# Kernel optimization log

Hardware: AMD Instinct MI355X
Metric: run time of the kernel (lower is better)

The kernel has to match this reference:

```python
import jax, jax.numpy as jnp
import numpy as np

DIM = 2048
INTER = 1408          # moe_inter_dim per routed expert
N_EXPERTS = 32
TOPK = 6
N_GROUPS = 8
TOPK_GROUPS = 4
ROUTE_SCALE = 2.5
SHARED_INTER = 2816   # n_shared_experts(2) * moe_inter_dim
T = 8192              # tokens (batch*seq flattened)
INIT = 0.02


def setup_inputs() -> dict:
    key = jax.random.key(0)
    k = jax.random.split(key, 8)
    x = jax.random.normal(k[0], (T, DIM), jnp.float32)
    gate_w = jax.random.normal(k[1], (N_EXPERTS, DIM), jnp.float32) * INIT
    # stacked routed-expert weights (torch Linear convention: [out, in])
    w1 = jax.random.normal(k[2], (N_EXPERTS, INTER, DIM), jnp.float32) * INIT
    w2 = jax.random.normal(k[3], (N_EXPERTS, DIM, INTER), jnp.float32) * INIT
    w3 = jax.random.normal(k[4], (N_EXPERTS, INTER, DIM), jnp.float32) * INIT
    # shared experts (single fused MLP, inter = n_shared * moe_inter_dim)
    sw1 = jax.random.normal(k[5], (SHARED_INTER, DIM), jnp.float32) * INIT
    sw2 = jax.random.normal(k[6], (DIM, SHARED_INTER), jnp.float32) * INIT
    sw3 = jax.random.normal(k[7], (SHARED_INTER, DIM), jnp.float32) * INIT
    return {"x": x, "gate_w": gate_w, "w1": w1, "w2": w2, "w3": w3,
            "sw1": sw1, "sw2": sw2, "sw3": sw3}


def _gate(x, gate_w):
    # sigmoid scores, no bias (dim != 7168), group-limited top-k routing
    scores = jax.nn.sigmoid(x @ gate_w.T)                  # (T, E)
    original = scores
    sg = scores.reshape(x.shape[0], N_GROUPS, -1)          # (T, G, E/G)
    group_scores = sg.max(axis=-1)                         # (T, G)  (amax branch)
    _, gidx = jax.lax.top_k(group_scores, TOPK_GROUPS)     # (T, Gk)
    gmask = jnp.zeros((x.shape[0], N_GROUPS), bool).at[
        jnp.arange(x.shape[0])[:, None], gidx].set(True)
    masked = jnp.where(gmask[:, :, None], sg, 0.0).reshape(x.shape[0], -1)
    _, idx = jax.lax.top_k(masked, TOPK)                   # (T, K)
    w = jnp.take_along_axis(original, idx, axis=1)         # gather pre-mask scores
    w = w / w.sum(axis=-1, keepdims=True)                  # sigmoid normalization
    w = w * ROUTE_SCALE
    return w.astype(x.dtype), idx


def reference(x, gate_w, w1, w2, w3, sw1, sw2, sw3):
    weights, idx = _gate(x, gate_w)                        # (T,K), (T,K) int
    # per-token combine weight for each expert: cw[t,e] = sum_k w[t,k]*[idx==e]
    onehot = jax.nn.one_hot(idx, N_EXPERTS, dtype=weights.dtype)  # (T,K,E)
    cw = jnp.einsum('tk,tke->et', weights, onehot)         # (E, T)

    def expert_step(acc, ew):
        W1, W2, W3, cwe = ew                               # cwe: (T,)
        h = jax.nn.silu(x @ W1.T) * (x @ W3.T)             # (T, INTER)
        return acc + cwe[:, None] * (h @ W2.T), None

    y, _ = jax.lax.scan(expert_step, jnp.zeros_like(x), (w1, w2, w3, cw))
    # shared experts MLP (SwiGLU)
    z = (jax.nn.silu(x @ sw1.T) * (x @ sw3.T)) @ sw2.T
    return y + z
```

## Files before the change

### kernel.cpp

```cpp
#include <hip/hip_runtime.h>
#include <hip/hip_bf16.h>
#include <stdint.h>

typedef unsigned short u16;

#define T_TOK 8192
#define DIM 2048
#define INTER 1408
#define NEXP 32
#define TOPK 6
#define SHINTER 2816
#define SLOTS (T_TOK * TOPK)

typedef __attribute__((ext_vector_type(8))) short bf16x8;
typedef __attribute__((ext_vector_type(4))) float f32x4;

__device__ inline u16 f2bf(float f) {
  union { float f; unsigned u; } c; c.f = f;
  unsigned r = (c.u + 0x7FFFu + ((c.u >> 16) & 1u)) >> 16;
  return (u16)r;
}
__device__ inline float bf2f(u16 h) {
  union { unsigned u; float f; } c; c.u = ((unsigned)h) << 16;
  return c.f;
}

__device__ __forceinline__ void gl16(const void* g, void* l) {
  __builtin_amdgcn_global_load_lds(
      (const __attribute__((address_space(1))) void*)g,
      (__attribute__((address_space(3))) void*)l, 16, 0, 0);
}

__global__ __launch_bounds__(256)
void gate_route_k(const float* __restrict__ x, const float* __restrict__ gw,
                  int* __restrict__ tidx, float* __restrict__ tw, int* __restrict__ counts)
{
  int lane = threadIdx.x & 63, w = threadIdx.x >> 6;
  int t = blockIdx.x * 4 + w;
  __shared__ float sc[4][32];
  __shared__ float gm[4][8];
  const float* xr = x + (size_t)t * DIM + lane * 4;
  float4 xv[8];
#pragma unroll
  for (int i = 0; i < 8; i++) xv[i] = *(const float4*)(xr + i * 256);
  for (int e = 0; e < NEXP; e++) {
    const float* g = gw + (size_t)e * DIM + lane * 4;
    float acc = 0.f;
#pragma unroll
    for (int i = 0; i < 8; i++) {
      float4 gv = *(const float4*)(g + i * 256);
      acc += xv[i].x * gv.x + xv[i].y * gv.y + xv[i].z * gv.z + xv[i].w * gv.w;
    }
#pragma unroll
    for (int off = 32; off > 0; off >>= 1) acc += __shfl_down(acc, off);
    if (lane == 0) sc[w][e] = 1.f / (1.f + __expf(-acc));
  }
  if (lane == 0) {
#pragma unroll
    for (int g = 0; g < 8; g++)
      gm[w][g] = fmaxf(fmaxf(sc[w][g*4+0], sc[w][g*4+1]), fmaxf(sc[w][g*4+2], sc[w][g*4+3]));
    unsigned gsel = 0u;
    for (int it = 0; it < 4; it++) {
      float best = -1.f; int bi = 0;
      for (int g = 0; g < 8; g++)
        if (!((gsel >> g) & 1u) && gm[w][g] > best) { best = gm[w][g]; bi = g; }
      gsel |= 1u << bi;
    }
    unsigned chosen = 0u; float wsum = 0.f;
    int ids[TOPK]; float wv[TOPK];
#pragma unroll
    for (int it = 0; it < TOPK; it++) {
      float best = -1.f; int bi = 0;
      for (int e = 0; e < NEXP; e++)
        if (((gsel >> (e >> 2)) & 1u) && !((chosen >> e) & 1u) && sc[w][e] > best) { best = sc[w][e]; bi = e; }
      chosen |= 1u << bi; ids[it] = bi; wv[it] = best; wsum += best;
    }
    float s = 2.5f / wsum;
#pragma unroll
    for (int k = 0; k < TOPK; k++) {
      tidx[t * TOPK + k] = ids[k];
      tw[t * TOPK + k] = wv[k] * s;
      atomicAdd(&counts[ids[k]], 1);
    }
  }
}

__global__ void zero32(int* p) { if (threadIdx.x < NEXP) p[threadIdx.x] = 0; }

__global__ void scan_desc_k(const int* __restrict__ counts, int* __restrict__ offs,
                            int4* __restrict__ desc, int* __restrict__ ntiles)
{
  if (threadIdx.x != 0 || blockIdx.x != 0) return;
  int off = 0, n = 0;
  for (int e = 0; e < NEXP; e++) {
    offs[e] = off;
    int c = counts[e];
    int nt = (c + 127) >> 7;
    for (int i = 0; i < nt; i++) {
      int rem = c - i * 128;
      desc[n] = make_int4(e, off + i * 128, rem < 128 ? rem : 128, 0);
      n++;
    }
    off += c;
  }
  offs[NEXP] = off;
  ntiles[0] = n;
}

__global__ __launch_bounds__(256)
void perm_build_k(const int* __restrict__ tidx, const float* __restrict__ tw,
                  const int* __restrict__ offs, int* __restrict__ ptok,
                  float* __restrict__ pw, int* __restrict__ slotof)
{
  int e = blockIdx.x;
  int tid = threadIdx.x, lane = tid & 63, w = tid >> 6;
  __shared__ int wsum[4];
  __shared__ int cursor;
  if (tid == 0) cursor = offs[e];
  __syncthreads();
  for (int start = 0; start < SLOTS; start += 256) {
    int i = start + tid;
    int match = (tidx[i] == e) ? 1 : 0;
    unsigned long long b = __ballot(match);
    if (lane == 0) wsum[w] = __popcll(b);
    __syncthreads();
    int base = cursor;
    int waveoff = 0;
    for (int ww = 0; ww < w; ww++) waveoff += wsum[ww];
    int total = wsum[0] + wsum[1] + wsum[2] + wsum[3];
    if (match) {
      int before = __popcll(b & ((1ull << lane) - 1ull));
      int slot = base + waveoff + before;
      ptok[slot] = i / TOPK;
      pw[slot] = tw[i];
      slotof[i] = slot;
    }
    __syncthreads();
    if (tid == 0) cursor = base + total;
  }
}

__global__ __launch_bounds__(256)
void cvt_w_k(const float* __restrict__ src, u16* __restrict__ dst, int n8)
{
  int stride = gridDim.x * 256;
  for (size_t i = (size_t)blockIdx.x * 256 + threadIdx.x; i < (size_t)n8; i += stride) {
    size_t j = i * 8;
    float4 a = *(const float4*)(src + j);
    float4 b = *(const float4*)(src + j + 4);
    union { u16 h[8]; uint4 u; } p;
    p.h[0] = f2bf(a.x); p.h[1] = f2bf(a.y); p.h[2] = f2bf(a.z); p.h[3] = f2bf(a.w);
    p.h[4] = f2bf(b.x); p.h[5] = f2bf(b.y); p.h[6] = f2bf(b.z); p.h[7] = f2bf(b.w);
    *(uint4*)(dst + j) = p.u;
  }
}


template<bool SHARED>
__global__ __launch_bounds__(256, 2)
void up2_k(const u16* __restrict__ xb,
           const u16* __restrict__ B1g, const u16* __restrict__ B3g,
           const int* __restrict__ ptok,
           const int4* __restrict__ desc, const int* __restrict__ ntiles,
           u16* __restrict__ Hout)
{
  constexpr int HLD = SHARED ? SHINTER : INTER;
  int row_tile = blockIdx.x, col_tile = blockIdx.y;
  int slot_base, rows;
  const u16 *B1, *B3;
  if constexpr (SHARED) { slot_base = row_tile * 128; rows = 128; B1 = B1g; B3 = B3g; }
  else {
    if (row_tile >= ntiles[0]) return;
    int4 d = desc[row_tile];
    slot_base = d.y; rows = d.z;
    size_t off = (size_t)d.x * (size_t)INTER * DIM;
    B1 = B1g + off; B3 = B3g + off;
  }
  int n0 = col_tile * 128;
  int tid = threadIdx.x, lane = tid & 63;
  int w = tid >> 6, wr = w >> 1, wc = w & 1;

  __shared__ u16 As[128][64];
  __shared__ u16 Bs1[128][64];
  __shared__ u16 Bs3[128][64];

  int selem = (((lane & 7) ^ (lane >> 3)) * 8);
  const u16 *a_src[4], *b1_src[4], *b3_src[4];
#pragma unroll
  for (int s = 0; s < 4; s++) {
    int r = w * 32 + s * 8 + (lane >> 3);
    int tok;
    if constexpr (SHARED) tok = slot_base + r;
    else { int rr = r < rows ? r : rows - 1; tok = ptok[slot_base + rr]; }
    a_src[s]  = xb + (size_t)tok * DIM + selem;
    b1_src[s] = B1 + (size_t)(n0 + r) * DIM + selem;
    b3_src[s] = B3 + (size_t)(n0 + r) * DIM + selem;
  }

  f32x4 acc1[4][4], acc3[4][4];
#pragma unroll
  for (int m = 0; m < 4; m++)
#pragma unroll
    for (int n = 0; n < 4; n++) { acc1[m][n] = {0.f,0.f,0.f,0.f}; acc3[m][n] = {0.f,0.f,0.f,0.f}; }

  for (int kk = 0; kk < DIM / 64; kk++) {
    __syncthreads();
#pragma unroll
    for (int s = 0; s < 4; s++) {
      gl16(a_src[s]  + kk * 64, &As [w * 32 + s * 8][0]);
      gl16(b1_src[s] + kk * 64, &Bs1[w * 32 + s * 8][0]);
      gl16(b3_src[s] + kk * 64, &Bs3[w * 32 + s * 8][0]);
    }
    __syncthreads();
#pragma unroll
    for (int h = 0; h < 2; h++) {
      bf16x8 af[4], b1f[4], b3f[4];
      int chk = (h * 4 + (lane >> 4)) ^ (lane & 7);
#pragma unroll
      for (int m = 0; m < 4; m++)
        af[m] = *(const bf16x8*)&As[wr * 64 + m * 16 + (lane & 15)][chk * 8];
#pragma unroll
      for (int n = 0; n < 4; n++) {
        b1f[n] = *(const bf16x8*)&Bs1[wc * 64 + n * 16 + (lane & 15)][chk * 8];
        b3f[n] = *(const bf16x8*)&Bs3[wc * 64 + n * 16 + (lane & 15)][chk * 8];
      }
#pragma unroll
      for (int m = 0; m < 4; m++)
#pragma unroll
        for (int n = 0; n < 4; n++) {
          acc1[m][n] = __builtin_amdgcn_mfma_f32_16x16x32_bf16(af[m], b1f[n], acc1[m][n], 0, 0, 0);
          acc3[m][n] = __builtin_amdgcn_mfma_f32_16x16x32_bf16(af[m], b3f[n], acc3[m][n], 0, 0, 0);
        }
    }
  }
#pragma unroll
  for (int m = 0; m < 4; m++) {
#pragma unroll
    for (int r = 0; r < 4; r++) {
      int row_local = wr * 64 + m * 16 + (lane >> 4) * 4 + r;
      if (row_local < rows) {
        size_t rowp = (size_t)(slot_base + row_local) * HLD + n0 + wc * 64 + (lane & 15);
#pragma unroll
        for (int n = 0; n < 4; n++) {
          float c1 = acc1[m][n][r], c3 = acc3[m][n][r];
          float hval = (c1 / (1.f + __expf(-c1))) * c3;
          Hout[rowp + n * 16] = f2bf(hval);
        }
      }
    }
  }
}

template<bool SHARED>
__global__ __launch_bounds__(256, 2)
void down2_k(const u16* __restrict__ Hin, const u16* __restrict__ Bg,
             const int4* __restrict__ desc, const int* __restrict__ ntiles,
             const float* __restrict__ pw,
             u16* __restrict__ slotout, float* __restrict__ yout)
{
  constexpr int KD = SHARED ? SHINTER : INTER;
  constexpr int KSTEPS = KD / 64;
  int row_tile = blockIdx.x, col_tile = blockIdx.y;
  int slot_base, rows; const u16* B;
  if constexpr (SHARED) { slot_base = row_tile * 128; rows = 128; B = Bg; }
  else {
    if (row_tile >= ntiles[0]) return;
    int4 d = desc[row_tile]; slot_base = d.y; rows = d.z;
    B = Bg + (size_t)d.x * DIM * INTER;
  }
  int n0 = col_tile * 128;
  int tid = threadIdx.x, lane = tid & 63;
  int w = tid >> 6, wr = w >> 1, wc = w & 1;
  __shared__ u16 As[128][64];
  __shared__ u16 Bs[128][64];

  int selem = (((lane & 7) ^ (lane >> 3)) * 8);
  const u16 *a_src[4], *b_src[4];
#pragma unroll
  for (int s = 0; s < 4; s++) {
    int r = w * 32 + s * 8 + (lane >> 3);
    a_src[s] = Hin + (size_t)(slot_base + r) * KD + selem;
    b_src[s] = B + (size_t)(n0 + r) * KD + selem;
  }

  f32x4 acc[4][4];
#pragma unroll
  for (int m = 0; m < 4; m++)
#pragma unroll
    for (int n = 0; n < 4; n++) acc[m][n] = {0.f,0.f,0.f,0.f};

  for (int kk = 0; kk < KSTEPS; kk++) {
    __syncthreads();
#pragma unroll
    for (int s = 0; s < 4; s++) {
      gl16(a_src[s] + kk * 64, &As[w * 32 + s * 8][0]);
      gl16(b_src[s] + kk * 64, &Bs[w * 32 + s * 8][0]);
    }
    __syncthreads();
#pragma unroll
    for (int h = 0; h < 2; h++) {
      bf16x8 af[4], bfv[4];
      int chk = (h * 4 + (lane >> 4)) ^ (lane & 7);
#pragma unroll
      for (int m = 0; m < 4; m++)
        af[m] = *(const bf16x8*)&As[wr * 64 + m * 16 + (lane & 15)][chk * 8];
#pragma unroll
      for (int n = 0; n < 4; n++)
        bfv[n] = *(const bf16x8*)&Bs[wc * 64 + n * 16 + (lane & 15)][chk * 8];
#pragma unroll
      for (int m = 0; m < 4; m++)
#pragma unroll
        for (int n = 0; n < 4; n++)
          acc[m][n] = __builtin_amdgcn_mfma_f32_16x16x32_bf16(af[m], bfv[n], acc[m][n], 0, 0, 0);
    }
  }
#pragma unroll
  for (int m = 0; m < 4; m++) {
#pragma unroll
    for (int r = 0; r < 4; r++) {
      int row_local = wr * 64 + m * 16 + (lane >> 4) * 4 + r;
      if (row_local < rows) {
        int slot = slot_base + row_local;
        size_t rp = (size_t)slot * DIM + n0 + wc * 64 + (lane & 15);
        if constexpr (SHARED) {
#pragma unroll
          for (int n = 0; n < 4; n++) yout[rp + n * 16] = acc[m][n][r];
        } else {
          float sw = pw[slot];
#pragma unroll
          for (int n = 0; n < 4; n++) slotout[rp + n * 16] = f2bf(acc[m][n][r] * sw);
        }
      }
    }
  }
}

template<bool SHARED>
__global__ __launch_bounds__(256, 2)
void up_gemm_k(const u16* __restrict__ xb,
               const float* __restrict__ W1g, const float* __restrict__ W3g,
               const int* __restrict__ ptok,
               const int4* __restrict__ desc, const int* __restrict__ ntiles,
               u16* __restrict__ Hout)
{
  constexpr int HLD = SHARED ? SHINTER : INTER;
  int row_tile = blockIdx.x, col_tile = blockIdx.y;
  int slot_base, rows;
  const float *B1, *B3;
  if constexpr (SHARED) {
    slot_base = row_tile * 128; rows = 128; B1 = W1g; B3 = W3g;
  } else {
    if (row_tile >= ntiles[0]) return;
    int4 d = desc[row_tile];
    slot_base = d.y; rows = d.z;
    size_t off = (size_t)d.x * (size_t)INTER * DIM;
    B1 = W1g + off; B3 = W3g + off;
  }
  int n0 = col_tile * 128;
  int tid = threadIdx.x, lane = tid & 63;
  int wv = tid >> 6, wr = wv >> 1, wc = wv & 1;

  __shared__ u16 As[128][72];
  __shared__ u16 Bs1[128][72];
  __shared__ u16 Bs3[128][72];

  int ar = tid >> 3, ac = (tid & 7) * 8;
  const u16* asrc[4];
#pragma unroll
  for (int s = 0; s < 4; s++) {
    int r = s * 32 + ar;
    int tok;
    if constexpr (SHARED) tok = slot_base + r;
    else { int rr = r < rows ? r : rows - 1; tok = ptok[slot_base + rr]; }
    asrc[s] = xb + (size_t)tok * DIM + ac;
  }
  int br = tid >> 4, bc = (tid & 15) * 4;
  const float* b1p = B1 + (size_t)(n0 + br) * DIM + bc;
  const float* b3p = B3 + (size_t)(n0 + br) * DIM + bc;

  f32x4 acc1[4][4], acc3[4][4];
#pragma unroll
  for (int m = 0; m < 4; m++)
#pragma unroll
    for (int n = 0; n < 4; n++) { acc1[m][n] = {0.f,0.f,0.f,0.f}; acc3[m][n] = {0.f,0.f,0.f,0.f}; }

  for (int kk = 0; kk < DIM / 64; kk++) {
    __syncthreads();
#pragma unroll
    for (int s = 0; s < 4; s++) {
      uint4 v = *(const uint4*)(asrc[s] + kk * 64);
      *(uint4*)&As[s * 32 + ar][ac] = v;
    }
#pragma unroll
    for (int s = 0; s < 8; s++) {
      float4 v = *(const float4*)(b1p + (size_t)(s * 16) * DIM + kk * 64);
      union { u16 h[4]; uint2 q; } o;
      o.h[0] = f2bf(v.x); o.h[1] = f2bf(v.y); o.h[2] = f2bf(v.z); o.h[3] = f2bf(v.w);
      *(uint2*)&Bs1[s * 16 + br][bc] = o.q;
    }
#pragma unroll
    for (int s = 0; s < 8; s++) {
      float4 v = *(const float4*)(b3p + (size_t)(s * 16) * DIM + kk * 64);
      union { u16 h[4]; uint2 q; } o;
      o.h[0] = f2bf(v.x); o.h[1] = f2bf(v.y); o.h[2] = f2bf(v.z); o.h[3] = f2bf(v.w);
      *(uint2*)&Bs3[s * 16 + br][bc] = o.q;
    }
    __syncthreads();
#pragma unroll
    for (int h = 0; h < 2; h++) {
      bf16x8 af[4], b1f[4], b3f[4];
#pragma unroll
      for (int m = 0; m < 4; m++)
        af[m] = *(const bf16x8*)&As[wr * 64 + m * 16 + (lane & 15)][h * 32 + (lane >> 4) * 8];
#pragma unroll
      for (int n = 0; n < 4; n++) {
        b1f[n] = *(const bf16x8*)&Bs1[wc * 64 + n * 16 + (lane & 15)][h * 32 + (lane >> 4) * 8];
        b3f[n] = *(const bf16x8*)&Bs3[wc * 64 + n * 16 + (lane & 15)][h * 32 + (lane >> 4) * 8];
      }
#pragma unroll
      for (int m = 0; m < 4; m++)
#pragma unroll
        for (int n = 0; n < 4; n++) {
          acc1[m][n] = __builtin_amdgcn_mfma_f32_16x16x32_bf16(af[m], b1f[n], acc1[m][n], 0, 0, 0);
          acc3[m][n] = __builtin_amdgcn_mfma_f32_16x16x32_bf16(af[m], b3f[n], acc3[m][n], 0, 0, 0);
        }
    }
  }
#pragma unroll
  for (int m = 0; m < 4; m++) {
#pragma unroll
    for (int r = 0; r < 4; r++) {
      int row_local = wr * 64 + m * 16 + (lane >> 4) * 4 + r;
      if (row_local < rows) {
        size_t rowp = (size_t)(slot_base + row_local) * HLD + n0 + wc * 64 + (lane & 15);
#pragma unroll
        for (int n = 0; n < 4; n++) {
          float c1 = acc1[m][n][r], c3 = acc3[m][n][r];
          float hval = (c1 / (1.f + __expf(-c1))) * c3;
          Hout[rowp + n * 16] = f2bf(hval);
        }
      }
    }
  }
}

template<bool SHARED>
__global__ __launch_bounds__(256, 2)
void down_gemm_k(const u16* __restrict__ Hin, const float* __restrict__ Bg,
                 const int4* __restrict__ desc, const int* __restrict__ ntiles,
                 const float* __restrict__ pw,
                 u16* __restrict__ slotout, float* __restrict__ yout)
{
  constexpr int KD = SHARED ? SHINTER : INTER;
  constexpr int KSTEPS = KD / 64;
  int row_tile = blockIdx.x, col_tile = blockIdx.y;
  int slot_base, rows; const float* B;
  if constexpr (SHARED) { slot_base = row_tile * 128; rows = 128; B = Bg; }
  else {
    if (row_tile >= ntiles[0]) return;
    int4 d = desc[row_tile]; slot_base = d.y; rows = d.z;
    B = Bg + (size_t)d.x * DIM * INTER;
  }
  int n0 = col_tile * 128;
  int tid = threadIdx.x, lane = tid & 63;
  int wv = tid >> 6, wr = wv >> 1, wc = wv & 1;
  __shared__ u16 As[128][72];
  __shared__ u16 Bs[128][72];
  int ar = tid >> 3, ac = (tid & 7) * 8;
  const u16* asrc[4];
#pragma unroll
  for (int s = 0; s < 4; s++)
    asrc[s] = Hin + (size_t)(slot_base + s * 32 + ar) * KD + ac;
  int br = tid >> 4, bc = (tid & 15) * 4;
  const float* bp = B + (size_t)(n0 + br) * KD + bc;

  f32x4 acc[4][4];
#pragma unroll
  for (int m = 0; m < 4; m++)
#pragma unroll
    for (int n = 0; n < 4; n++) acc[m][n] = {0.f,0.f,0.f,0.f};

  for (int kk = 0; kk < KSTEPS; kk++) {
    __syncthreads();
#pragma unroll
    for (int s = 0; s < 4; s++) {
      uint4 v = *(const uint4*)(asrc[s] + kk * 64);
      *(uint4*)&As[s * 32 + ar][ac] = v;
    }
#pragma unroll
    for (int s = 0; s < 8; s++) {
      float4 v = *(const float4*)(bp + (size_t)(s * 16) * KD + kk * 64);
      union { u16 h[4]; uint2 q; } o;
      o.h[0] = f2bf(v.x); o.h[1] = f2bf(v.y); o.h[2] = f2bf(v.z); o.h[3] = f2bf(v.w);
      *(uint2*)&Bs[s * 16 + br][bc] = o.q;
    }
    __syncthreads();
#pragma unroll
    for (int h = 0; h < 2; h++) {
      bf16x8 af[4], bfv[4];
#pragma unroll
      for (int m = 0; m < 4; m++)
        af[m] = *(const bf16x8*)&As[wr * 64 + m * 16 + (lane & 15)][h * 32 + (lane >> 4) * 8];
#pragma unroll
      for (int n = 0; n < 4; n++)
        bfv[n] = *(const bf16x8*)&Bs[wc * 64 + n * 16 + (lane & 15)][h * 32 + (lane >> 4) * 8];
#pragma unroll
      for (int m = 0; m < 4; m++)
#pragma unroll
        for (int n = 0; n < 4; n++)
          acc[m][n] = __builtin_amdgcn_mfma_f32_16x16x32_bf16(af[m], bfv[n], acc[m][n], 0, 0, 0);
    }
  }
#pragma unroll
  for (int m = 0; m < 4; m++) {
#pragma unroll
    for (int r = 0; r < 4; r++) {
      int row_local = wr * 64 + m * 16 + (lane >> 4) * 4 + r;
      if (row_local < rows) {
        int slot = slot_base + row_local;
        size_t rp = (size_t)slot * DIM + n0 + wc * 64 + (lane & 15);
        if constexpr (SHARED) {
#pragma unroll
          for (int n = 0; n < 4; n++) yout[rp + n * 16] = acc[m][n][r];
        } else {
          float sw = pw[slot];
#pragma unroll
          for (int n = 0; n < 4; n++) slotout[rp + n * 16] = f2bf(acc[m][n][r] * sw);
        }
      }
    }
  }
}

__global__ __launch_bounds__(256)
void combine_k(float* __restrict__ y, const u16* __restrict__ slotout, const int* __restrict__ slotof)
{
  int t = blockIdx.x;
  int c = threadIdx.x * 8;
  size_t rp = (size_t)t * DIM + c;
  float4 a = *(const float4*)(y + rp);
  float4 b = *(const float4*)(y + rp + 4);
  float o[8] = {a.x, a.y, a.z, a.w, b.x, b.y, b.z, b.w};
#pragma unroll
  for (int k = 0; k < TOPK; k++) {
    int s = slotof[t * TOPK + k];
    uint4 v = *(const uint4*)(slotout + (size_t)s * DIM + c);
    o[0] += bf2f((u16)(v.x & 0xFFFFu)); o[1] += bf2f((u16)(v.x >> 16));
    o[2] += bf2f((u16)(v.y & 0xFFFFu)); o[3] += bf2f((u16)(v.y >> 16));
    o[4] += bf2f((u16)(v.z & 0xFFFFu)); o[5] += bf2f((u16)(v.z >> 16));
    o[6] += bf2f((u16)(v.w & 0xFFFFu)); o[7] += bf2f((u16)(v.w >> 16));
  }
  *(float4*)(y + rp)     = make_float4(o[0], o[1], o[2], o[3]);
  *(float4*)(y + rp + 4) = make_float4(o[4], o[5], o[6], o[7]);
}

extern "C" void kernel_launch(void* const* d_in, const int* in_sizes, int n_in,
                              void* d_out, int out_size, void* d_ws, size_t ws_size,
                              hipStream_t stream)
{
  const float* x   = (const float*)d_in[0];
  const float* gw  = (const float*)d_in[1];
  const float* w1  = (const float*)d_in[2];
  const float* w2  = (const float*)d_in[3];
  const float* w3  = (const float*)d_in[4];
  const float* sw1 = (const float*)d_in[5];
  const float* sw2 = (const float*)d_in[6];
  const float* sw3 = (const float*)d_in[7];
  float* y = (float*)d_out;
  char* ws = (char*)d_ws;

  int*   counts = (int*)(ws + 0);
  int*   ntiles = (int*)(ws + 256);
  int*   offs   = (int*)(ws + 512);
  int4*  desc   = (int4*)(ws + 768);
  int*   tidx   = (int*)(ws + 8192);
  float* tw     = (float*)(ws + 204800);
  int*   ptok   = (int*)(ws + 401408);
  float* pw     = (float*)(ws + 598016);
  int*   slotof = (int*)(ws + 794624);
  u16*   xb     = (u16*)(ws + 991232);
  u16*   H      = (u16*)(ws + 34545664ull);
  u16*   Hs     = (u16*)(ws + 173318144ull);
  u16*   sout   = (u16*)(ws + 219455488ull);
  u16*   w1b    = (u16*)(ws + 420782080ull);
  u16*   w3b    = (u16*)(ws + 605331456ull);
  u16*   w2b    = (u16*)(ws + 789880832ull);
  u16*   sw1b   = (u16*)(ws + 974430208ull);
  u16*   sw3b   = (u16*)(ws + 985964544ull);
  u16*   sw2b   = (u16*)(ws + 997498880ull);
  const unsigned long long NEED_FULL = 1009033216ull;

  zero32<<<1, 64, 0, stream>>>(counts);
  gate_route_k<<<2048, 256, 0, stream>>>(x, gw, tidx, tw, counts);
  cvt_w_k<<<2048, 256, 0, stream>>>(x, xb, T_TOK * DIM / 8);
  scan_desc_k<<<1, 64, 0, stream>>>(counts, offs, desc, ntiles);
  perm_build_k<<<32, 256, 0, stream>>>(tidx, tw, offs, ptok, pw, slotof);

  if (ws_size >= NEED_FULL) {
    const int NW = NEXP * INTER * DIM / 8;
    const int NS = SHINTER * DIM / 8;
    cvt_w_k<<<4096, 256, 0, stream>>>(w1,  w1b,  NW);
    cvt_w_k<<<4096, 256, 0, stream>>>(w3,  w3b,  NW);
    cvt_w_k<<<4096, 256, 0, stream>>>(w2,  w2b,  NW);
    cvt_w_k<<<1024, 256, 0, stream>>>(sw1, sw1b, NS);
    cvt_w_k<<<1024, 256, 0, stream>>>(sw3, sw3b, NS);
    cvt_w_k<<<1024, 256, 0, stream>>>(sw2, sw2b, NS);

    up2_k<false><<<dim3(416, 11), 256, 0, stream>>>(xb, w1b, w3b, ptok, desc, ntiles, H);
    up2_k<true ><<<dim3(64, 22), 256, 0, stream>>>(xb, sw1b, sw3b, ptok, desc, ntiles, Hs);
    down2_k<true ><<<dim3(64, 16), 256, 0, stream>>>(Hs, sw2b, desc, ntiles, pw, sout, y);
    down2_k<false><<<dim3(416, 16), 256, 0, stream>>>(H, w2b, desc, ntiles, pw, sout, y);
  } else {
    up_gemm_k<false><<<dim3(416, 11), 256, 0, stream>>>(xb, w1, w3, ptok, desc, ntiles, H);
    up_gemm_k<true ><<<dim3(64, 22), 256, 0, stream>>>(xb, sw1, sw3, ptok, desc, ntiles, Hs);
    down_gemm_k<true ><<<dim3(64, 16), 256, 0, stream>>>(Hs, sw2, desc, ntiles, pw, sout, y);
    down_gemm_k<false><<<dim3(416, 16), 256, 0, stream>>>(H, w2, desc, ntiles, pw, sout, y);
  }

  combine_k<<<8192, 256, 0, stream>>>(y, sout, slotof);
}
```

Measured before the change: 2.487 ms.

## Parallelize scan, widen perm build, raise GEMM occupancy, remap row tiles across XCDs

The expert-offset scan moves from one serial thread to wave-wide shuffle prefix sums, and the permutation builder uses 1024-thread blocks. The grouped GEMM kernels raise the launch-bounds occupancy hint from 2 to 3 blocks per CU. They also permute blockIdx.x so that consecutive row tiles land on the same XCD, with the aim of improving L2 reuse of expert weights. The higher occupancy hint may force register spills, and the tile remap relies on gridDim.x being divisible by 8.

```diff
diff --git a/kernel.cpp b/kernel.cpp
--- a/kernel.cpp
+++ b/kernel.cpp
@@ -88,37 +88,50 @@
 __global__ void zero32(int* p) { if (threadIdx.x < NEXP) p[threadIdx.x] = 0; }
 
 __global__ void scan_desc_k(const int* __restrict__ counts, int* __restrict__ offs,
-                            int4* __restrict__ desc, int* __restrict__ ntiles)
-{
-  if (threadIdx.x != 0 || blockIdx.x != 0) return;
-  int off = 0, n = 0;
-  for (int e = 0; e < NEXP; e++) {
-    offs[e] = off;
-    int c = counts[e];
-    int nt = (c + 127) >> 7;
+                            int4* __restrict__ desc128, int* __restrict__ ntiles)
+{
+  int lane = threadIdx.x;
+  int c = (lane < NEXP) ? counts[lane] : 0;
+  int inc = c;
+#pragma unroll
+  for (int d = 1; d < 64; d <<= 1) {
+    int v = __shfl_up(inc, d);
+    if (lane >= d) inc += v;
+  }
+  int off_e = inc - c;
+  int nt = (c + 127) >> 7;
+  int tinc = nt;
+#pragma unroll
+  for (int d = 1; d < 64; d <<= 1) {
+    int v = __shfl_up(tinc, d);
+    if (lane >= d) tinc += v;
+  }
+  int tex = tinc - nt;
+  if (lane < NEXP) {
+    offs[lane] = off_e;
     for (int i = 0; i < nt; i++) {
       int rem = c - i * 128;
-      desc[n] = make_int4(e, off + i * 128, rem < 128 ? rem : 128, 0);
-      n++;
-    }
-    off += c;
-  }
-  offs[NEXP] = off;
-  ntiles[0] = n;
-}
-
-__global__ __launch_bounds__(256)
+      desc128[tex + i] = make_int4(lane, off_e + i * 128, rem < 128 ? rem : 128, 0);
+    }
+  }
+  if (lane == NEXP - 1) {
+    offs[NEXP] = inc;
+    ntiles[0] = tinc;
+  }
+}
+
+__global__ __launch_bounds__(1024)
 void perm_build_k(const int* __restrict__ tidx, const float* __restrict__ tw,
                   const int* __restrict__ offs, int* __restrict__ ptok,
                   float* __restrict__ pw, int* __restrict__ slotof)
 {
   int e = blockIdx.x;
   int tid = threadIdx.x, lane = tid & 63, w = tid >> 6;
-  __shared__ int wsum[4];
+  __shared__ int wsum[16];
   __shared__ int cursor;
   if (tid == 0) cursor = offs[e];
   __syncthreads();
-  for (int start = 0; start < SLOTS; start += 256) {
+  for (int start = 0; start < SLOTS; start += 1024) {
     int i = start + tid;
     int match = (tidx[i] == e) ? 1 : 0;
     unsigned long long b = __ballot(match);
@@ -127,7 +140,9 @@
     int base = cursor;
     int waveoff = 0;
     for (int ww = 0; ww < w; ww++) waveoff += wsum[ww];
-    int total = wsum[0] + wsum[1] + wsum[2] + wsum[3];
+    int total = 0;
+#pragma unroll
+    for (int ww = 0; ww < 16; ww++) total += wsum[ww];
     if (match) {
       int before = __popcll(b & ((1ull << lane) - 1ull));
       int slot = base + waveoff + before;
@@ -157,7 +172,7 @@
 
 
 template<bool SHARED>
-__global__ __launch_bounds__(256, 2)
+__global__ __launch_bounds__(256, 3)
 void up2_k(const u16* __restrict__ xb,
            const u16* __restrict__ B1g, const u16* __restrict__ B3g,
            const int* __restrict__ ptok,
@@ -165,7 +180,9 @@
            u16* __restrict__ Hout)
 {
   constexpr int HLD = SHARED ? SHINTER : INTER;
-  int row_tile = blockIdx.x, col_tile = blockIdx.y;
+  int rt0 = blockIdx.x;
+  int row_tile = (rt0 & 7) * (int)(gridDim.x >> 3) + (rt0 >> 3);
+  int col_tile = blockIdx.y;
   int slot_base, rows;
   const u16 *B1, *B3;
   if constexpr (SHARED) { slot_base = row_tile * 128; rows = 128; B1 = B1g; B3 = B3g; }
@@ -252,7 +269,7 @@
 }
 
 template<bool SHARED>
-__global__ __launch_bounds__(256, 2)
+__global__ __launch_bounds__(256, 3)
 void down2_k(const u16* __restrict__ Hin, const u16* __restrict__ Bg,
              const int4* __restrict__ desc, const int* __restrict__ ntiles,
              const float* __restrict__ pw,
@@ -260,7 +277,9 @@
 {
   constexpr int KD = SHARED ? SHINTER : INTER;
   constexpr int KSTEPS = KD / 64;
-  int row_tile = blockIdx.x, col_tile = blockIdx.y;
+  int rt0 = blockIdx.x;
+  int row_tile = (rt0 & 7) * (int)(gridDim.x >> 3) + (rt0 >> 3);
+  int col_tile = blockIdx.y;
   int slot_base, rows; const u16* B;
   if constexpr (SHARED) { slot_base = row_tile * 128; rows = 128; B = Bg; }
   else {
@@ -569,32 +588,32 @@
   float* y = (float*)d_out;
   char* ws = (char*)d_ws;
 
-  int*   counts = (int*)(ws + 0);
-  int*   ntiles = (int*)(ws + 256);
-  int*   offs   = (int*)(ws + 512);
-  int4*  desc   = (int4*)(ws + 768);
-  int*   tidx   = (int*)(ws + 8192);
-  float* tw     = (float*)(ws + 204800);
-  int*   ptok   = (int*)(ws + 401408);
-  float* pw     = (float*)(ws + 598016);
-  int*   slotof = (int*)(ws + 794624);
-  u16*   xb     = (u16*)(ws + 991232);
-  u16*   H      = (u16*)(ws + 34545664ull);
-  u16*   Hs     = (u16*)(ws + 173318144ull);
-  u16*   sout   = (u16*)(ws + 219455488ull);
-  u16*   w1b    = (u16*)(ws + 420782080ull);
-  u16*   w3b    = (u16*)(ws + 605331456ull);
-  u16*   w2b    = (u16*)(ws + 789880832ull);
-  u16*   sw1b   = (u16*)(ws + 974430208ull);
-  u16*   sw3b   = (u16*)(ws + 985964544ull);
-  u16*   sw2b   = (u16*)(ws + 997498880ull);
-  const unsigned long long NEED_FULL = 1009033216ull;
+  int*   counts  = (int*)(ws + 0);
+  int*   ntiles  = (int*)(ws + 256);
+  int*   offs    = (int*)(ws + 512);
+  int4*  desc128 = (int4*)(ws + 1024);
+  int*   tidx    = (int*)(ws + 16384);
+  float* tw      = (float*)(ws + 212992);
+  int*   ptok    = (int*)(ws + 409600);
+  float* pw      = (float*)(ws + 606208);
+  int*   slotof  = (int*)(ws + 802816);
+  u16*   xb      = (u16*)(ws + 1048576);
+  u16*   H       = (u16*)(ws + 34603008ull);
+  u16*   Hs      = (u16*)(ws + 173735936ull);
+  u16*   sout    = (u16*)(ws + 219873280ull);
+  u16*   w1b     = (u16*)(ws + 421199872ull);
+  u16*   w3b     = (u16*)(ws + 605749248ull);
+  u16*   w2b     = (u16*)(ws + 790298624ull);
+  u16*   sw1b    = (u16*)(ws + 974848000ull);
+  u16*   sw3b    = (u16*)(ws + 986382336ull);
+  u16*   sw2b    = (u16*)(ws + 997916672ull);
+  const unsigned long long NEED_FULL = 1009451008ull;
 
   zero32<<<1, 64, 0, stream>>>(counts);
   gate_route_k<<<2048, 256, 0, stream>>>(x, gw, tidx, tw, counts);
   cvt_w_k<<<2048, 256, 0, stream>>>(x, xb, T_TOK * DIM / 8);
-  scan_desc_k<<<1, 64, 0, stream>>>(counts, offs, desc, ntiles);
-  perm_build_k<<<32, 256, 0, stream>>>(tidx, tw, offs, ptok, pw, slotof);
+  scan_desc_k<<<1, 64, 0, stream>>>(counts, offs, desc128, ntiles);
+  perm_build_k<<<32, 1024, 0, stream>>>(tidx, tw, offs, ptok, pw, slotof);
 
   if (ws_size >= NEED_FULL) {
     const int NW = NEXP * INTER * DIM / 8;
@@ -606,15 +625,15 @@
     cvt_w_k<<<1024, 256, 0, stream>>>(sw3, sw3b, NS);
     cvt_w_k<<<1024, 256, 0, stream>>>(sw2, sw2b, NS);
 
-    up2_k<false><<<dim3(416, 11), 256, 0, stream>>>(xb, w1b, w3b, ptok, desc, ntiles, H);
-    up2_k<true ><<<dim3(64, 22), 256, 0, stream>>>(xb, sw1b, sw3b, ptok, desc, ntiles, Hs);
-    down2_k<true ><<<dim3(64, 16), 256, 0, stream>>>(Hs, sw2b, desc, ntiles, pw, sout, y);
-    down2_k<false><<<dim3(416, 16), 256, 0, stream>>>(H, w2b, desc, ntiles, pw, sout, y);
+    up2_k<false><<<dim3(416, 11), 256, 0, stream>>>(xb, w1b, w3b, ptok, desc128, ntiles, H);
+    up2_k<true ><<<dim3(64, 22), 256, 0, stream>>>(xb, sw1b, sw3b, ptok, desc128, ntiles, Hs);
+    down2_k<true ><<<dim3(64, 16), 256, 0, stream>>>(Hs, sw2b, desc128, ntiles, pw, sout, y);
+    down2_k<false><<<dim3(416, 16), 256, 0, stream>>>(H, w2b, desc128, ntiles, pw, sout, y);
   } else {
-    up_gemm_k<false><<<dim3(416, 11), 256, 0, stream>>>(xb, w1, w3, ptok, desc, ntiles, H);
-    up_gemm_k<true ><<<dim3(64, 22), 256, 0, stream>>>(xb, sw1, sw3, ptok, desc, ntiles, Hs);
-    down_gemm_k<true ><<<dim3(64, 16), 256, 0, stream>>>(Hs, sw2, desc, ntiles, pw, sout, y);
-    down_gemm_k<false><<<dim3(416, 16), 256, 0, stream>>>(H, w2, desc, ntiles, pw, sout, y);
+    up_gemm_k<false><<<dim3(416, 11), 256, 0, stream>>>(xb, w1, w3, ptok, desc128, ntiles, H);
+    up_gemm_k<true ><<<dim3(64, 22), 256, 0, stream>>>(xb, sw1, sw3, ptok, desc128, ntiles, Hs);
+    down_gemm_k<true ><<<dim3(64, 16), 256, 0, stream>>>(Hs, sw2, desc128, ntiles, pw, sout, y);
+    down_gemm_k<false><<<dim3(416, 16), 256, 0, stream>>>(H, w2, desc128, ntiles, pw, sout, y);
   }
 
   combine_k<<<8192, 256, 0, stream>>>(y, sout, slotof);
```

Result: slower. 3.740 ms (+50.4%).
